# Performance work log

Hardware: AMD Instinct MI355X
Metric: run time of the kernel (lower is better)

The kernel has to match this reference:

```python
import jax, jax.numpy as jnp
import numpy as np

LEAK = 0.95
NUM_STEPS = 10
THR = 1.0  # all layers get threshold = 1.0 in __init__

@jax.custom_vjp
def spike(x):
    # Surrogate_BP_Function.forward: heaviside(x > 0)
    return (x > 0).astype(x.dtype)

def _spike_fwd(x):
    return spike(x), x

def _spike_bwd(x, g):
    # backward: grad * 0.3 * relu(1 - |x|)
    return (g * 0.3 * jnp.maximum(1.0 - jnp.abs(x), 0.0),)

spike.defvjp(_spike_fwd, _spike_bwd)

def conv3x3(x, w):
    # stride 1, padding 1, no bias, NCHW / OIHW
    return jax.lax.conv_general_dilated(
        x, w, window_strides=(1, 1), padding=[(1, 1), (1, 1)],
        dimension_numbers=('NCHW', 'OIHW', 'NCHW'))

def avgpool2(x):
    b, c, h, w = x.shape
    return x.reshape(b, c, h // 2, 2, w // 2, 2).mean(axis=(3, 5))

def setup_inputs() -> dict:
    key = jax.random.key(0)
    ks = jax.random.split(key, 11)
    def w(k, shape, scale):
        return jax.random.normal(k, shape, dtype=jnp.float32) * scale
    inp = jax.random.normal(ks[0], (128, 3, 32, 32), dtype=jnp.float32)
    return {
        'inp': inp,
        'w1': w(ks[1], (64, 3, 3, 3), 0.35),
        'w2': w(ks[2], (64, 64, 3, 3), 0.1),
        'w3': w(ks[3], (128, 64, 3, 3), 0.1),
        'w4': w(ks[4], (128, 128, 3, 3), 0.08),
        'w5': w(ks[5], (256, 128, 3, 3), 0.08),
        'w6': w(ks[6], (256, 256, 3, 3), 0.06),
        'w7': w(ks[7], (256, 256, 3, 3), 0.06),
        'fc1_w': w(ks[8], (1024, 4096), 0.03),   # Linear(4*4*256, 1024)
        'fc2_w': w(ks[9], (10, 1024), 0.05),     # Linear(1024, 10)
    }

def reference(inp, w1, w2, w3, w4, w5, w6, w7, fc1_w, fc2_w):
    batch = inp.shape[0]
    conv_ws = [w2, w3, w4, w5, w6, w7]          # layers i = 1..6
    pool_after = [True, False, True, False, False, True]  # pool1 after i=1, pool2 after i=3, pool3 after i=6
    static = conv3x3(inp, w1)                   # static_input = conv1(inp)

    def step(carry, _):
        mem0, mem_fc1, mem_fc2 = carry
        # LIF update for conv1 (leaky accumulation of static input)
        mem0 = (1.0 - LEAK) * mem0 + LEAK * static
        thr = mem0 / THR - 1.0
        out_prev = spike(thr)
        mem0 = mem0 - jnp.where(thr > 0, THR, 0.0)  # soft reset
        # conv layers 2..7: membrane is OVERWRITTEN by the conv output each step
        for j, w in enumerate(conv_ws):
            m = conv3x3(out_prev, w)
            thr = m / THR - 1.0
            out_prev = spike(thr)
            if pool_after[j]:
                out_prev = avgpool2(out_prev)
        flat = out_prev.reshape(batch, -1)      # [B, 256*4*4]
        mem_fc1 = (1.0 - LEAK) * mem_fc1 + LEAK * (flat @ fc1_w.T)
        thr = mem_fc1 / THR - 1.0
        out = spike(thr)
        mem_fc1 = mem_fc1 - jnp.where(thr > 0, THR, 0.0)
        mem_fc2 = mem_fc2 + out @ fc2_w.T
        return (mem0, mem_fc1, mem_fc2), None

    init = (jnp.zeros_like(static),
            jnp.zeros((batch, 1024), dtype=inp.dtype),
            jnp.zeros((batch, fc2_w.shape[0]), dtype=inp.dtype))
    (mem0, mem_fc1, mem_fc2), _ = jax.lax.scan(step, init, None, length=NUM_STEPS)
    return mem_fc2 / NUM_STEPS
```

## Files before the change

kernel.cpp:

```cpp
#include <hip/hip_runtime.h>


typedef __attribute__((ext_vector_type(4))) int int32x4;

__device__ __forceinline__ float bf2f(ushort h) {
    union { unsigned u; float f; } v; v.u = ((unsigned)h) << 16;
    return v.f;
}
constexpr int ilog2(int x) { int r = 0; while (x > 1) { x >>= 1; ++r; } return r; }

__device__ __forceinline__ void gl_lds16(const void* g, void* l) {
    __builtin_amdgcn_global_load_lds(
        (const __attribute__((address_space(1))) unsigned int*)g,
        (__attribute__((address_space(3))) unsigned int*)l, 16, 0, 0);
}

#define SC21 4.76837158203125e-07
#define SC23 1.1920928955078125e-07

template <int IC, int OC>
__global__ void prep_convw_i8_k(const float* __restrict__ w, char* __restrict__ dst) {
    int idx = blockIdx.x * 256 + threadIdx.x;
    if (idx >= OC * IC * 9) return;
    int oc = idx / (IC * 9);
    int rem = idx % (IC * 9);
    int ic = rem / 9, q = rem % 9;
    int wq_ = (int)rintf(w[idx] * 2097152.0f);
    int a2 = ((wq_ + 128) & 255) - 128;
    int t2 = (wq_ - a2) >> 8;
    int a1 = ((t2 + 128) & 255) - 128;
    int a0 = (t2 - a1) >> 8;
    int sg = ic >> 6, kin = ic & 63, c = kin >> 4, bb = kin & 15;
    int oct = oc >> 6, ocl = oc & 63;
    constexpr int OCT = OC / 64;
    size_t base = ((size_t)(sg * 9 + q) * OCT + oct) * 12288;
    char digs[3] = {(char)a0, (char)a1, (char)a2};
#pragma unroll
    for (int s = 0; s < 3; ++s)
        dst[base + (size_t)(c * 192 + s * 64 + ocl) * 16 + bb] = digs[s];
}

__global__ void prep_fc1w_i8_k(const float* __restrict__ w, char* __restrict__ dst) {
    int idx = blockIdx.x * 256 + threadIdx.x;
    if (idx >= 1024 * 4096) return;
    int j = idx >> 12, k = idx & 4095;
    int c = k >> 4, hw = k & 15;
    int kp = hw * 256 + c;
    int wq_ = (int)rintf(w[idx] * 2097152.0f);
    int a2 = ((wq_ + 128) & 255) - 128;
    int t2 = (wq_ - a2) >> 8;
    int a1 = ((t2 + 128) & 255) - 128;
    int a0 = (t2 - a1) >> 8;
    int slab = kp >> 6, kin = kp & 63, cch = kin >> 4, bb = kin & 15;
    int oct = j >> 6, ocl = j & 63;
    size_t base = ((size_t)(slab * 16 + oct)) * 12288;
    char digs[3] = {(char)a0, (char)a1, (char)a2};
#pragma unroll
    for (int s = 0; s < 3; ++s)
        dst[base + (size_t)(cch * 192 + s * 64 + ocl) * 16 + bb] = digs[s];
}

template <int H, int C>
__global__ void halo0_k(char* __restrict__ buf) {
    constexpr int P = 4 * H + 4;
    constexpr int CPI = P * (C / 16);
    int idx = blockIdx.x * 256 + threadIdx.x;
    if (idx >= 1280 * CPI) return;
    int n = idx / CPI, r = idx % CPI;
    int p = r / (C / 16), c16 = r % (C / 16);
    int row, col;
    if (p < 2 * (H + 2)) { row = (p < H + 2) ? 0 : H + 1; col = p % (H + 2); }
    else { int qq = p - 2 * (H + 2); col = (qq < H) ? 0 : H + 1; row = 1 + (qq % H); }
    *(uint4*)&buf[(((size_t)n * (H + 2) + row) * (H + 2) + col) * C + c16 * 16] =
        (uint4){0u, 0u, 0u, 0u};
}

__global__ __launch_bounds__(256) void conv1lif_k(const float* __restrict__ inp,
                                                  const float* __restrict__ w1,
                                                  char* __restrict__ act1) {
    __shared__ float ws[27 * 64];
    for (int e = threadIdx.x; e < 1728; e += 256) {
        int oc = e / 27, j = e % 27;
        ws[j * 64 + oc] = w1[e];
    }
    __syncthreads();
    int t = blockIdx.x * 256 + threadIdx.x;
    int q = t & 3;
    int m = t >> 2;
    int n = m >> 10, h = (m >> 5) & 31, w = m & 31;
    float xv[27];
#pragma unroll
    for (int ic = 0; ic < 3; ++ic)
#pragma unroll
        for (int kh = 0; kh < 3; ++kh)
#pragma unroll
            for (int kw = 0; kw < 3; ++kw) {
                int r = h + kh - 1, c = w + kw - 1;
                xv[ic * 9 + kh * 3 + kw] =
                    (r >= 0 && r < 32 && c >= 0 && c < 32)
                        ? inp[(n * 3 + ic) * 1024 + r * 32 + c] : 0.0f;
            }
    float s[16], mem[16];
#pragma unroll
    for (int o = 0; o < 16; ++o) { s[o] = 0.f; mem[o] = 0.f; }
#pragma unroll
    for (int j = 0; j < 27; ++j) {
        float x = xv[j];
        const float* wr = &ws[j * 64 + q * 16];
#pragma unroll
        for (int o = 0; o < 16; ++o) s[o] += wr[o] * x;
    }
    const size_t dbase = (((size_t)h + 1) * 34 + (w + 1)) * 64 + q * 16;
    for (int st = 0; st < 10; ++st) {
        unsigned r[4];
#pragma unroll
        for (int g = 0; g < 4; ++g) {
            unsigned acc = 0;
#pragma unroll
            for (int e = 0; e < 4; ++e) {
                int o = g * 4 + e;
                mem[o] = 0.05f * mem[o] + 0.95f * s[o];
                unsigned b = (mem[o] > 1.f) ? 1u : 0u;
                mem[o] -= (float)b;
                acc |= b << (8 * e);
            }
            r[g] = acc;
        }
        size_t d = ((size_t)(st * 128 + n) * 34 * 34) * 64 + dbase;
        *(uint4*)&act1[d] = (uint4){r[0], r[1], r[2], r[3]};
    }
}

template <int H, int W, int IC, int OC, int NI, int MR, int EPI>
__global__ __launch_bounds__(512) void convi8_k(const char* __restrict__ act,
                                                const char* __restrict__ wq,
                                                char* __restrict__ outs,
                                                float scale) {
    constexpr int PW = W + 2, PHR = MR + 2;
    constexpr int MBLK = NI * MR * W;
    constexpr int NPIX = NI * PHR * PW;
    constexpr int ACH = NPIX * 4;
    constexpr int HR = (ACH + 511) / 512;
    constexpr int SLABS = IC / 64;
    constexpr int OCT = OC / 64;
    constexpr int U = SLABS * 9;
    constexpr int LHW = ilog2(H * W), LW2 = ilog2(W), LMW = ilog2(MR * W);
    static_assert(MBLK == 256, "tile mapping");

    __shared__ __align__(16) char sA[NPIX * 64];
    __shared__ __align__(16) char sB[2][12288];

    const int tid = threadIdx.x, lane = tid & 63;
    const int wid = tid >> 6;
    const int wm = wid >> 1, wn = wid & 1;
    const int b = blockIdx.x, oct = blockIdx.y;
    const int oc0 = oct * 64;
    const int m0 = b * MBLK;
    constexpr int TPI = (NI == 1) ? (H / MR) : 1;
    const int n0 = (NI == 1) ? (b / TPI) : (b * NI);
    const int h0 = (NI == 1) ? (b % TPI) * MR : 0;

    int asrc[HR]; bool apred[HR];
#pragma unroll
    for (int r = 0; r < HR; ++r) {
        int i = r * 512 + tid;
        apred[r] = (i < ACH);
        int ii = apred[r] ? i : 0;
        int c = ii / NPIX, pix = ii % NPIX;
        int pc = pix % PW, t2 = pix / PW;
        int hp = t2 % PHR, img = t2 / PHR;
        asrc[r] = (((n0 + img) * (H + 2) + h0 + hp) * PW + pc) * IC + c * 16;
    }
    int apix[4];
#pragma unroll
    for (int am = 0; am < 4; ++am) {
        int p = wm * 64 + am * 16 + (lane & 15);
        int img = p >> LMW;
        int pi = p & ((MR * W) - 1);
        int h = pi >> LW2;
        apix[am] = (img * PHR + h) * PW + (pi & (W - 1));
    }
    const int cA = lane >> 4;
    const int lan15 = lane & 15;

    int32x4 acc[3][4][2];
#pragma unroll
    for (int s = 0; s < 3; ++s)
#pragma unroll
        for (int a = 0; a < 4; ++a)
#pragma unroll
            for (int bn = 0; bn < 2; ++bn) acc[s][a][bn] = (int32x4){0, 0, 0, 0};

    const size_t wqoct = (size_t)oct * 12288;

    auto stage_B = [&](int unit, int bufc) {
        const char* wsrc = wq + (size_t)unit * (OCT * 12288) + wqoct;
        gl_lds16(wsrc + tid * 16, sB[bufc] + tid * 16);
        if (tid < 256)
            gl_lds16(wsrc + 8192 + tid * 16, sB[bufc] + 8192 + tid * 16);
    };
    auto stage_A = [&](int sl_) {
#pragma unroll
        for (int r = 0; r < HR; ++r)
            if (apred[r]) gl_lds16(act + asrc[r] + sl_ * 64, sA + (r * 512 + tid) * 16);
    };

    stage_A(0);
    stage_B(0, 0);
    __syncthreads();

    int buf = 0;
    for (int sl = 0; sl < SLABS; ++sl) {
#pragma unroll
        for (int q = 0; q < 9; ++q) {
            const int u = sl * 9 + q;
            if (u + 1 < U) stage_B(u + 1, buf ^ 1);
            const int qr = q / 3, qc = q - qr * 3;
            int32x4 af[4];
#pragma unroll
            for (int am = 0; am < 4; ++am)
                af[am] = *(const int32x4*)&sA[(cA * NPIX + apix[am] + qr * PW + qc) * 16];
            __builtin_amdgcn_s_setprio(1);
#pragma unroll
            for (int s = 0; s < 3; ++s)
#pragma unroll
                for (int bn = 0; bn < 2; ++bn) {
                    int R = s * 64 + wn * 32 + bn * 16 + lan15;
                    int32x4 bf = *(const int32x4*)&sB[buf][(cA * 192 + R) * 16];
#pragma unroll
                    for (int am = 0; am < 4; ++am)
                        acc[s][am][bn] = __builtin_amdgcn_mfma_i32_16x16x64_i8(
                            af[am], bf, acc[s][am][bn], 0, 0, 0);
                }
            __builtin_amdgcn_s_setprio(0);
            __syncthreads();
            buf ^= 1;
        }
        if (sl + 1 < SLABS) {
            stage_A(sl + 1);
            __syncthreads();
        }
    }

#pragma unroll
    for (int am = 0; am < 4; ++am)
#pragma unroll
        for (int bn = 0; bn < 2; ++bn)
#pragma unroll
            for (int rr = 0; rr < 4; ++rr) {
                int rl = wm * 64 + am * 16 + (lane >> 4) * 4 + rr;
                int col = oc0 + wn * 32 + bn * 16 + (lane & 15);
                int m = m0 + rl;
                float v = (float)((65536.0 * (double)acc[0][am][bn][rr]
                                 + 256.0 * (double)acc[1][am][bn][rr]
                                 + (double)acc[2][am][bn][rr]) * (double)scale);
                char sp = (v > 1.0f) ? (char)1 : (char)0;
                if (EPI == 1) {
                    int n = m >> LHW, h = (m >> LW2) & (H - 1), w = m & (W - 1);
                    outs[((size_t)(n * (H + 2) + h + 1) * PW + (w + 1)) * OC + col] = sp;
                } else {
                    outs[(size_t)m * OC + col] = sp;
                }
            }
}

template <int C, int HI>
__global__ void pool_i8_k(const char* __restrict__ in, char* __restrict__ out) {
    constexpr int HO = HI / 2, C16 = C / 16;
    constexpr int TOT = 1280 * HO * HO * C16;
    int idx = blockIdx.x * 256 + threadIdx.x;
    if (idx >= TOT) return;
    int c16 = idx % C16;
    int t = idx / C16;
    int w = t % HO; t /= HO;
    int h = t % HO;
    int n = t / HO;
    const char* p = in + ((size_t)(n * HI + 2 * h) * HI + 2 * w) * C + c16 * 16;
    uint4 a0 = *(const uint4*)p;
    uint4 a1 = *(const uint4*)(p + C);
    uint4 a2 = *(const uint4*)(p + (size_t)HI * C);
    uint4 a3 = *(const uint4*)(p + (size_t)HI * C + C);
    uint4 r;
    r.x = a0.x + a1.x + a2.x + a3.x;
    r.y = a0.y + a1.y + a2.y + a3.y;
    r.z = a0.z + a1.z + a2.z + a3.z;
    r.w = a0.w + a1.w + a2.w + a3.w;
    *(uint4*)&out[((size_t)(n * (HO + 2) + h + 1) * (HO + 2) + (w + 1)) * C + c16 * 16] = r;
}

__global__ void pool3q_k(const char* __restrict__ in, char* __restrict__ out) {
    int idx = blockIdx.x * 256 + threadIdx.x;
    if (idx >= 327680) return;
    int c16 = idx & 15;
    int t = idx >> 4;
    int wo = t & 3, ho = (t >> 2) & 3, n = t >> 4;
    const char* p = in + ((size_t)(n * 8 + 2 * ho) * 8 + 2 * wo) * 256 + c16 * 16;
    uint4 a0 = *(const uint4*)p;
    uint4 a1 = *(const uint4*)(p + 256);
    uint4 a2 = *(const uint4*)(p + 2048);
    uint4 a3 = *(const uint4*)(p + 2048 + 256);
    uint4 r;
    r.x = a0.x + a1.x + a2.x + a3.x;
    r.y = a0.y + a1.y + a2.y + a3.y;
    r.z = a0.z + a1.z + a2.z + a3.z;
    r.w = a0.w + a1.w + a2.w + a3.w;
    *(uint4*)&out[((size_t)(n * 16 + ho * 4 + wo) * 16 + c16) * 16] = r;
}

__global__ __launch_bounds__(256) void fc1i8_k(const char* __restrict__ A,
                                               const char* __restrict__ wq,
                                               float* __restrict__ part) {
    __shared__ __align__(16) char sA[2][8192];
    __shared__ __align__(16) char sB[2][12288];
    const int tid = threadIdx.x, lane = tid & 63;
    const int wid = tid >> 6, wm = wid >> 1, wn = wid & 1;
    const int m0 = blockIdx.x * 128, oct = blockIdx.y, kt = blockIdx.z;

    int32x4 acc[3][4][2];
#pragma unroll
    for (int s = 0; s < 3; ++s)
#pragma unroll
        for (int a = 0; a < 4; ++a)
#pragma unroll
            for (int bn = 0; bn < 2; ++bn) acc[s][a][bn] = (int32x4){0, 0, 0, 0};

    auto stageA = [&](int sg, int bf_) {
#pragma unroll
        for (int r = 0; r < 2; ++r) {
            int i = r * 256 + tid;
            int c = i >> 7, pix = i & 127;
            gl_lds16(A + (size_t)(m0 + pix) * 4096 + sg * 64 + c * 16,
                     sA[bf_] + (size_t)i * 16);
        }
    };
    auto stageB = [&](int sg, int bf_) {
        const char* src = wq + ((size_t)(sg * 16 + oct)) * 12288 + tid * 16;
#pragma unroll
        for (int r = 0; r < 3; ++r)
            gl_lds16(src + r * 4096, sB[bf_] + (r * 256 + tid) * 16);
    };

    int buf = 0;
    stageA(kt * 32, 0);
    stageB(kt * 32, 0);
    __syncthreads();
    const int cA = lane >> 4;
    for (int sl = 0; sl < 32; ++sl) {
        int sg = kt * 32 + sl;
        if (sl < 31) { stageA(sg + 1, buf ^ 1); stageB(sg + 1, buf ^ 1); }
        int32x4 af[4];
#pragma unroll
        for (int am = 0; am < 4; ++am)
            af[am] = *(const int32x4*)&sA[buf][(cA * 128 + wm * 64 + am * 16 + (lane & 15)) * 16];
#pragma unroll
        for (int s = 0; s < 3; ++s)
#pragma unroll
            for (int bn = 0; bn < 2; ++bn) {
                int R = s * 64 + wn * 32 + bn * 16 + (lane & 15);
                int32x4 bf = *(const int32x4*)&sB[buf][(cA * 192 + R) * 16];
#pragma unroll
                for (int am = 0; am < 4; ++am)
                    acc[s][am][bn] = __builtin_amdgcn_mfma_i32_16x16x64_i8(
                        af[am], bf, acc[s][am][bn], 0, 0, 0);
            }
        if (sl < 31) { __syncthreads(); buf ^= 1; }
    }
#pragma unroll
    for (int am = 0; am < 4; ++am)
#pragma unroll
        for (int bn = 0; bn < 2; ++bn)
#pragma unroll
            for (int rr = 0; rr < 4; ++rr) {
                int row = m0 + wm * 64 + am * 16 + (lane >> 4) * 4 + rr;
                int col = oct * 64 + wn * 32 + bn * 16 + (lane & 15);
                float v = (float)((65536.0 * (double)acc[0][am][bn][rr]
                                 + 256.0 * (double)acc[1][am][bn][rr]
                                 + (double)acc[2][am][bn][rr]) * SC23);
                part[((size_t)kt * 1280 + row) * 1024 + col] = v;
            }
}

__global__ void fc1lif_k(const float* __restrict__ part, ushort* __restrict__ sbuf) {
    int idx = blockIdx.x * 256 + threadIdx.x;
    int n = idx >> 10, j = idx & 1023;
    float m = 0.f;
    for (int t = 0; t < 10; ++t) {
        size_t row = (size_t)(t * 128 + n) * 1024 + j;
        float y = part[row] + part[1310720 + row];
        m = 0.05f * m + 0.95f * y;
        float sp = (m > 1.f) ? 1.f : 0.f;
        m -= sp;
        sbuf[row] = sp > 0.f ? (ushort)0x3F80 : (ushort)0;
    }
}

__global__ __launch_bounds__(256) void fc2o_k(const ushort* __restrict__ S,
                                              const float* __restrict__ W2,
                                              float* __restrict__ out) {
    __shared__ float wsh[10 * 1024];
    __shared__ float red[10][256];
    int n = blockIdx.x, tid = threadIdx.x;
    for (int e = tid; e < 10240; e += 256) wsh[e] = W2[e];
    __syncthreads();
    float accv = 0.f;
    for (int t = 0; t < 10; ++t) {
        const ushort* sp = S + ((size_t)(t * 128 + n)) * 1024 + tid * 4;
        float s0 = bf2f(sp[0]), s1 = bf2f(sp[1]), s2 = bf2f(sp[2]), s3 = bf2f(sp[3]);
#pragma unroll
        for (int o = 0; o < 10; ++o) {
            const float* w = &wsh[o * 1024 + tid * 4];
            red[o][tid] = s0 * w[0] + s1 * w[1] + s2 * w[2] + s3 * w[3];
        }
        __syncthreads();
        for (int off = 128; off >= 1; off >>= 1) {
            if (tid < off) {
#pragma unroll
                for (int o = 0; o < 10; ++o) red[o][tid] += red[o][tid + off];
            }
            __syncthreads();
        }
        if (tid < 10) accv += red[tid][0];
        __syncthreads();
    }
    if (tid < 10) out[n * 10 + tid] = accv * 0.1f;
}

extern "C" void kernel_launch(void* const* d_in, const int* in_sizes, int n_in,
                              void* d_out, int out_size, void* d_ws, size_t ws_size,
                              hipStream_t stream) {
    const float* inp  = (const float*)d_in[0];
    const float* w1   = (const float*)d_in[1];
    const float* w2   = (const float*)d_in[2];
    const float* w3   = (const float*)d_in[3];
    const float* w4   = (const float*)d_in[4];
    const float* w5   = (const float*)d_in[5];
    const float* w6   = (const float*)d_in[6];
    const float* w7   = (const float*)d_in[7];
    const float* fc1w = (const float*)d_in[8];
    const float* fc2w = (const float*)d_in[9];
    float* out = (float*)d_out;

    char* base = (char*)d_ws;
    char* arenaA = base;
    char* arenaB = base + 94679040;
    size_t o = 94679040 + 83886080;
    auto alloc = [&](size_t bytes) { void* p = base + o; o += (bytes + 255) & ~(size_t)255; return p; };
    char*   wq2  = (char*)alloc(110592);
    char*   wq3  = (char*)alloc(221184);
    char*   wq4  = (char*)alloc(442368);
    char*   wq5  = (char*)alloc(884736);
    char*   wq6  = (char*)alloc(1769472);
    char*   wq7  = (char*)alloc(1769472);
    char*   wqf1 = (char*)alloc(12582912);
    ushort* sbuf = (ushort*)alloc(2621440);
    (void)ws_size;

    char*  act1  = arenaA;
    char*  c2out = arenaB;
    char*  act2  = arenaA;
    char*  c3out = arenaB;
    char*  c4out = arenaA;
    char*  act3  = arenaA + 41943040;
    char*  c5out = arenaB;
    char*  c6out = arenaB + 33554432;
    char*  c7out = arenaA;
    char*  afc1  = arenaA + 20971520;
    float* part  = (float*)(arenaA + 26214400);

    prep_convw_i8_k<64, 64>  <<<(36864 + 255) / 256, 256, 0, stream>>>(w2, wq2);
    prep_convw_i8_k<64, 128> <<<(73728 + 255) / 256, 256, 0, stream>>>(w3, wq3);
    prep_convw_i8_k<128, 128><<<(147456 + 255) / 256, 256, 0, stream>>>(w4, wq4);
    prep_convw_i8_k<128, 256><<<(294912 + 255) / 256, 256, 0, stream>>>(w5, wq5);
    prep_convw_i8_k<256, 256><<<(589824 + 255) / 256, 256, 0, stream>>>(w6, wq6);
    prep_convw_i8_k<256, 256><<<(589824 + 255) / 256, 256, 0, stream>>>(w7, wq7);
    prep_fc1w_i8_k<<<(4194304 + 255) / 256, 256, 0, stream>>>(fc1w, wqf1);

    halo0_k<32, 64><<<(1280 * 132 * 4 + 255) / 256, 256, 0, stream>>>(act1);
    conv1lif_k<<<2048, 256, 0, stream>>>(inp, w1, act1);

    convi8_k<32, 32, 64, 64, 1, 8, 0>
        <<<dim3(5120, 1), 512, 0, stream>>>(act1, wq2, c2out, (float)SC21);
    halo0_k<16, 64><<<(1280 * 68 * 4 + 255) / 256, 256, 0, stream>>>(act2);
    pool_i8_k<64, 32><<<(1280 * 256 * 4 + 255) / 256, 256, 0, stream>>>(c2out, act2);

    halo0_k<16, 128><<<(1280 * 68 * 8 + 255) / 256, 256, 0, stream>>>(c3out);
    convi8_k<16, 16, 64, 128, 1, 16, 1>
        <<<dim3(1280, 2), 512, 0, stream>>>(act2, wq3, c3out, (float)SC23);
    convi8_k<16, 16, 128, 128, 1, 16, 0>
        <<<dim3(1280, 2), 512, 0, stream>>>(c3out, wq4, c4out, (float)SC21);
    halo0_k<8, 128><<<(1280 * 36 * 8 + 255) / 256, 256, 0, stream>>>(act3);
    pool_i8_k<128, 16><<<(1280 * 64 * 8 + 255) / 256, 256, 0, stream>>>(c4out, act3);

    halo0_k<8, 256><<<(1280 * 36 * 16 + 255) / 256, 256, 0, stream>>>(c5out);
    convi8_k<8, 8, 128, 256, 4, 8, 1>
        <<<dim3(320, 4), 512, 0, stream>>>(act3, wq5, c5out, (float)SC23);
    halo0_k<8, 256><<<(1280 * 36 * 16 + 255) / 256, 256, 0, stream>>>(c6out);
    convi8_k<8, 8, 256, 256, 4, 8, 1>
        <<<dim3(320, 4), 512, 0, stream>>>(c5out, wq6, c6out, (float)SC21);
    convi8_k<8, 8, 256, 256, 4, 8, 0>
        <<<dim3(320, 4), 512, 0, stream>>>(c6out, wq7, c7out, (float)SC21);

    pool3q_k<<<(327680 + 255) / 256, 256, 0, stream>>>(c7out, afc1);

    fc1i8_k<<<dim3(10, 16, 2), 256, 0, stream>>>(afc1, wqf1, part);
    fc1lif_k<<<512, 256, 0, stream>>>(part, sbuf);
    fc2o_k<<<128, 256, 0, stream>>>(sbuf, fc2w, out);
}
```

Baseline: 987.2 us.

## Shrink conv tiles to 64 pixels with 256-thread blocks and flatten slab loop

The int8 MFMA conv kernel moves from 512-thread blocks covering 256 output pixels to 256-thread blocks covering 64 pixels, with launch bounds of 4 blocks per CU. Grids grow fourfold and the per-wave accumulator footprint halves. The slab/tap double loop is also flattened into a single loop over units. The aim is more resident blocks and better latency hiding. In exchange, each block reloads the full weight slab for fewer pixels, so weight traffic per output rises and the halo overhead on activations grows.

```diff
diff --git a/kernel.cpp b/kernel.cpp
--- a/kernel.cpp
+++ b/kernel.cpp
@@ -132,27 +132,26 @@
 }
 
 template <int H, int W, int IC, int OC, int NI, int MR, int EPI>
-__global__ __launch_bounds__(512) void convi8_k(const char* __restrict__ act,
-                                                const char* __restrict__ wq,
-                                                char* __restrict__ outs,
-                                                float scale) {
+__global__ __launch_bounds__(256, 4) void convi8_k(const char* __restrict__ act,
+                                                   const char* __restrict__ wq,
+                                                   char* __restrict__ outs,
+                                                   float scale) {
     constexpr int PW = W + 2, PHR = MR + 2;
     constexpr int MBLK = NI * MR * W;
     constexpr int NPIX = NI * PHR * PW;
     constexpr int ACH = NPIX * 4;
-    constexpr int HR = (ACH + 511) / 512;
+    constexpr int HR = (ACH + 255) / 256;
     constexpr int SLABS = IC / 64;
     constexpr int OCT = OC / 64;
     constexpr int U = SLABS * 9;
     constexpr int LHW = ilog2(H * W), LW2 = ilog2(W), LMW = ilog2(MR * W);
-    static_assert(MBLK == 256, "tile mapping");
+    static_assert(MBLK == 64, "tile mapping");
 
     __shared__ __align__(16) char sA[NPIX * 64];
     __shared__ __align__(16) char sB[2][12288];
 
     const int tid = threadIdx.x, lane = tid & 63;
-    const int wid = tid >> 6;
-    const int wm = wid >> 1, wn = wid & 1;
+    const int wid = tid >> 6, wm = wid >> 1, wn = wid & 1;
     const int b = blockIdx.x, oct = blockIdx.y;
     const int oc0 = oct * 64;
     const int m0 = b * MBLK;
@@ -163,7 +162,7 @@
     int asrc[HR]; bool apred[HR];
 #pragma unroll
     for (int r = 0; r < HR; ++r) {
-        int i = r * 512 + tid;
+        int i = r * 256 + tid;
         apred[r] = (i < ACH);
         int ii = apred[r] ? i : 0;
         int c = ii / NPIX, pix = ii % NPIX;
@@ -171,38 +170,40 @@
         int hp = t2 % PHR, img = t2 / PHR;
         asrc[r] = (((n0 + img) * (H + 2) + h0 + hp) * PW + pc) * IC + c * 16;
     }
-    int apix[4];
-#pragma unroll
-    for (int am = 0; am < 4; ++am) {
-        int p = wm * 64 + am * 16 + (lane & 15);
+    const int lan15 = lane & 15;
+    int apix[2];
+#pragma unroll
+    for (int am = 0; am < 2; ++am) {
+        int p = wm * 32 + am * 16 + lan15;
         int img = p >> LMW;
         int pi = p & ((MR * W) - 1);
         int h = pi >> LW2;
         apix[am] = (img * PHR + h) * PW + (pi & (W - 1));
     }
     const int cA = lane >> 4;
-    const int lan15 = lane & 15;
-
-    int32x4 acc[3][4][2];
+
+    int32x4 acc[3][2][2];
 #pragma unroll
     for (int s = 0; s < 3; ++s)
 #pragma unroll
-        for (int a = 0; a < 4; ++a)
+        for (int a = 0; a < 2; ++a)
 #pragma unroll
             for (int bn = 0; bn < 2; ++bn) acc[s][a][bn] = (int32x4){0, 0, 0, 0};
 
     const size_t wqoct = (size_t)oct * 12288;
+    constexpr size_t USTRIDE = (size_t)OCT * 12288;
 
     auto stage_B = [&](int unit, int bufc) {
-        const char* wsrc = wq + (size_t)unit * (OCT * 12288) + wqoct;
-        gl_lds16(wsrc + tid * 16, sB[bufc] + tid * 16);
-        if (tid < 256)
-            gl_lds16(wsrc + 8192 + tid * 16, sB[bufc] + 8192 + tid * 16);
+        const char* wsrc = wq + (size_t)unit * USTRIDE + wqoct + tid * 16;
+        char* d = sB[bufc] + tid * 16;
+        gl_lds16(wsrc, d);
+        gl_lds16(wsrc + 4096, d + 4096);
+        gl_lds16(wsrc + 8192, d + 8192);
     };
     auto stage_A = [&](int sl_) {
 #pragma unroll
         for (int r = 0; r < HR; ++r)
-            if (apred[r]) gl_lds16(act + asrc[r] + sl_ * 64, sA + (r * 512 + tid) * 16);
+            if (apred[r]) gl_lds16(act + asrc[r] + sl_ * 64, sA + (r * 256 + tid) * 16);
     };
 
     stage_A(0);
@@ -210,46 +211,43 @@
     __syncthreads();
 
     int buf = 0;
-    for (int sl = 0; sl < SLABS; ++sl) {
-#pragma unroll
-        for (int q = 0; q < 9; ++q) {
-            const int u = sl * 9 + q;
-            if (u + 1 < U) stage_B(u + 1, buf ^ 1);
-            const int qr = q / 3, qc = q - qr * 3;
-            int32x4 af[4];
-#pragma unroll
-            for (int am = 0; am < 4; ++am)
-                af[am] = *(const int32x4*)&sA[(cA * NPIX + apix[am] + qr * PW + qc) * 16];
-            __builtin_amdgcn_s_setprio(1);
-#pragma unroll
-            for (int s = 0; s < 3; ++s)
-#pragma unroll
-                for (int bn = 0; bn < 2; ++bn) {
-                    int R = s * 64 + wn * 32 + bn * 16 + lan15;
-                    int32x4 bf = *(const int32x4*)&sB[buf][(cA * 192 + R) * 16];
-#pragma unroll
-                    for (int am = 0; am < 4; ++am)
-                        acc[s][am][bn] = __builtin_amdgcn_mfma_i32_16x16x64_i8(
-                            af[am], bf, acc[s][am][bn], 0, 0, 0);
-                }
-            __builtin_amdgcn_s_setprio(0);
-            __syncthreads();
-            buf ^= 1;
-        }
-        if (sl + 1 < SLABS) {
-            stage_A(sl + 1);
+    for (int u = 0; u < U; ++u) {
+        const int q = u - (u / 9) * 9;
+        if (u + 1 < U) stage_B(u + 1, buf ^ 1);
+        const int qr = q / 3, qc = q - qr * 3;
+        int32x4 af[2];
+#pragma unroll
+        for (int am = 0; am < 2; ++am)
+            af[am] = *(const int32x4*)&sA[(cA * NPIX + apix[am] + qr * PW + qc) * 16];
+        __builtin_amdgcn_s_setprio(1);
+#pragma unroll
+        for (int s = 0; s < 3; ++s)
+#pragma unroll
+            for (int bn = 0; bn < 2; ++bn) {
+                int R = s * 64 + wn * 32 + bn * 16 + lan15;
+                int32x4 bf = *(const int32x4*)&sB[buf][(cA * 192 + R) * 16];
+#pragma unroll
+                for (int am = 0; am < 2; ++am)
+                    acc[s][am][bn] = __builtin_amdgcn_mfma_i32_16x16x64_i8(
+                        af[am], bf, acc[s][am][bn], 0, 0, 0);
+            }
+        __builtin_amdgcn_s_setprio(0);
+        __syncthreads();
+        buf ^= 1;
+        if (q == 8 && u + 1 < U) {
+            stage_A(u / 9 + 1);
             __syncthreads();
         }
     }
 
 #pragma unroll
-    for (int am = 0; am < 4; ++am)
+    for (int am = 0; am < 2; ++am)
 #pragma unroll
         for (int bn = 0; bn < 2; ++bn)
 #pragma unroll
             for (int rr = 0; rr < 4; ++rr) {
-                int rl = wm * 64 + am * 16 + (lane >> 4) * 4 + rr;
-                int col = oc0 + wn * 32 + bn * 16 + (lane & 15);
+                int rl = wm * 32 + am * 16 + (lane >> 4) * 4 + rr;
+                int col = oc0 + wn * 32 + bn * 16 + lan15;
                 int m = m0 + rl;
                 float v = (float)((65536.0 * (double)acc[0][am][bn][rr]
                                  + 256.0 * (double)acc[1][am][bn][rr]
@@ -478,27 +476,27 @@
     halo0_k<32, 64><<<(1280 * 132 * 4 + 255) / 256, 256, 0, stream>>>(act1);
     conv1lif_k<<<2048, 256, 0, stream>>>(inp, w1, act1);
 
-    convi8_k<32, 32, 64, 64, 1, 8, 0>
-        <<<dim3(5120, 1), 512, 0, stream>>>(act1, wq2, c2out, (float)SC21);
+    convi8_k<32, 32, 64, 64, 1, 2, 0>
+        <<<dim3(20480, 1), 256, 0, stream>>>(act1, wq2, c2out, (float)SC21);
     halo0_k<16, 64><<<(1280 * 68 * 4 + 255) / 256, 256, 0, stream>>>(act2);
     pool_i8_k<64, 32><<<(1280 * 256 * 4 + 255) / 256, 256, 0, stream>>>(c2out, act2);
 
     halo0_k<16, 128><<<(1280 * 68 * 8 + 255) / 256, 256, 0, stream>>>(c3out);
-    convi8_k<16, 16, 64, 128, 1, 16, 1>
-        <<<dim3(1280, 2), 512, 0, stream>>>(act2, wq3, c3out, (float)SC23);
-    convi8_k<16, 16, 128, 128, 1, 16, 0>
-        <<<dim3(1280, 2), 512, 0, stream>>>(c3out, wq4, c4out, (float)SC21);
+    convi8_k<16, 16, 64, 128, 1, 4, 1>
+        <<<dim3(5120, 2), 256, 0, stream>>>(act2, wq3, c3out, (float)SC23);
+    convi8_k<16, 16, 128, 128, 1, 4, 0>
+        <<<dim3(5120, 2), 256, 0, stream>>>(c3out, wq4, c4out, (float)SC21);
     halo0_k<8, 128><<<(1280 * 36 * 8 + 255) / 256, 256, 0, stream>>>(act3);
     pool_i8_k<128, 16><<<(1280 * 64 * 8 + 255) / 256, 256, 0, stream>>>(c4out, act3);
 
     halo0_k<8, 256><<<(1280 * 36 * 16 + 255) / 256, 256, 0, stream>>>(c5out);
-    convi8_k<8, 8, 128, 256, 4, 8, 1>
-        <<<dim3(320, 4), 512, 0, stream>>>(act3, wq5, c5out, (float)SC23);
+    convi8_k<8, 8, 128, 256, 1, 8, 1>
+        <<<dim3(1280, 4), 256, 0, stream>>>(act3, wq5, c5out, (float)SC23);
     halo0_k<8, 256><<<(1280 * 36 * 16 + 255) / 256, 256, 0, stream>>>(c6out);
-    convi8_k<8, 8, 256, 256, 4, 8, 1>
-        <<<dim3(320, 4), 512, 0, stream>>>(c5out, wq6, c6out, (float)SC21);
-    convi8_k<8, 8, 256, 256, 4, 8, 0>
-        <<<dim3(320, 4), 512, 0, stream>>>(c6out, wq7, c7out, (float)SC21);
+    convi8_k<8, 8, 256, 256, 1, 8, 1>
+        <<<dim3(1280, 4), 256, 0, stream>>>(c5out, wq6, c6out, (float)SC21);
+    convi8_k<8, 8, 256, 256, 1, 8, 0>
+        <<<dim3(1280, 4), 256, 0, stream>>>(c6out, wq7, c7out, (float)SC21);
 
     pool3q_k<<<(327680 + 255) / 256, 256, 0, stream>>>(c7out, afc1);
 
```

Result: faster. 837.3 us (-15.2%).
